# Kernel optimization log

Hardware: AMD Instinct MI355X
Metric: run time of the kernel (lower is better)

Reference implementation:

```python
import jax, jax.numpy as jnp
import numpy as np

B, N, D, H, F = 2, 2048, 1024, 16, 4096
HD = D // H


def setup_inputs() -> dict:
    key = jax.random.key(0)
    ks = jax.random.split(key, 16)
    s = 0.02
    x = jax.random.normal(ks[0], (B, N, D), jnp.float32)
    # tail padding: lengths in [N//2, N]; position >= length is padded
    lengths = jax.random.randint(ks[1], (B,), N // 2, N + 1)
    key_padding_mask = jnp.arange(N)[None, :] >= lengths[:, None]  # [B,N] bool, True = pad
    return {
        "x": x,
        "key_padding_mask": key_padding_mask,
        "ln1_g": jnp.ones((D,), jnp.float32),
        "ln1_b": jnp.zeros((D,), jnp.float32),
        "w_in": jax.random.normal(ks[2], (3 * D, D), jnp.float32) * s,  # packed QKV in_proj
        "b_in": jnp.zeros((3 * D,), jnp.float32),
        "w_out": jax.random.normal(ks[3], (D, D), jnp.float32) * s,
        "b_out": jnp.zeros((D,), jnp.float32),
        "ln2_g": jnp.ones((D,), jnp.float32),
        "ln2_b": jnp.zeros((D,), jnp.float32),
        "w1": jax.random.normal(ks[4], (F, D), jnp.float32) * s,
        "b1": jnp.zeros((F,), jnp.float32),
        "w2": jax.random.normal(ks[5], (D, F), jnp.float32) * s,
        "b2": jnp.zeros((D,), jnp.float32),
    }


def _layernorm(x, g, b):
    # source LayerNorm forces fp32 then casts back
    xf = x.astype(jnp.float32)
    m = xf.mean(-1, keepdims=True)
    v = xf.var(-1, keepdims=True)
    return (((xf - m) * jax.lax.rsqrt(v + 1e-5)) * g + b).astype(x.dtype)


def _quick_gelu(x):
    return x * jax.nn.sigmoid(1.702 * x)


def _block(x, key_padding_mask, ln1_g, ln1_b, w_in, b_in, w_out, b_out,
           ln2_g, ln2_b, w1, b1, w2, b2):
    n = x.shape[1]
    # combined mask: causal OR key-pad, with diagonal unmasked for padded query rows
    causal = jnp.triu(jnp.ones((n, n), bool), 1)                      # [N,N]
    combined = causal[None] | key_padding_mask[:, None, :]            # [B,N,N]
    diag = jnp.eye(n, dtype=bool)
    combined = combined & ~(diag[None] & key_padding_mask[:, :, None])

    # --- attention (pre-norm) ---
    xn = _layernorm(x, ln1_g, ln1_b)
    qkv = xn @ w_in.T + b_in                                          # [B,N,3D]
    q, k, v = jnp.split(qkv, 3, axis=-1)
    def heads(t):
        return t.reshape(x.shape[0], n, H, HD).transpose(0, 2, 1, 3)  # [B,H,N,hd]
    q, k, v = heads(q), heads(k), heads(v)
    scores = jnp.einsum('bhqd,bhkd->bhqk', q, k) / np.sqrt(HD)        # [B,H,N,N]
    scores = jnp.where(combined[:, None], -jnp.inf, scores)
    probs = jax.nn.softmax(scores, axis=-1)                           # [B,H,N,N]
    attn = jnp.einsum('bhqk,bhkd->bqhd', probs, v).reshape(x.shape[0], n, D)
    attn = attn @ w_out.T + b_out
    attn = jnp.where(key_padding_mask[:, :, None], 0.0, attn)         # zero padded queries
    weights = probs.mean(axis=1)                                      # need_weights avg over heads

    x = x + attn
    # --- FFN (pre-norm) ---
    xn = _layernorm(x, ln2_g, ln2_b)
    mlp = _quick_gelu(xn @ w1.T + b1) @ w2.T + b2
    x = x + mlp
    return x, weights


def reference(x, key_padding_mask, ln1_g, ln1_b, w_in, b_in, w_out, b_out,
              ln2_g, ln2_b, w1, b1, w2, b2):
    return _block(x, key_padding_mask, ln1_g, ln1_b, w_in, b_in, w_out, b_out,
                  ln2_g, ln2_b, w1, b1, w2, b2)
```

## Files before the change

### kernel.cpp

```cpp
#include <hip/hip_runtime.h>
#include <hip/hip_bf16.h>
#include <stdint.h>

#define DEVI __device__ __forceinline__

typedef __attribute__((ext_vector_type(8)))  short bf16x8;
typedef __attribute__((ext_vector_type(4)))  short s16x4;
typedef __attribute__((ext_vector_type(4)))  float f32x4;
typedef __attribute__((ext_vector_type(16))) float f32x16;
typedef __attribute__((ext_vector_type(2)))  unsigned int u32x2;
typedef __attribute__((ext_vector_type(4)))  unsigned int u32x4;

#define L2E 1.44269504088896f

DEVI unsigned short f2bf(float f){
  union{float f; unsigned int u;} v; v.f = f;
  unsigned int u = v.u;
  u = u + 0x7FFFu + ((u >> 16) & 1u);
  return (unsigned short)(u >> 16);
}

DEVI unsigned int cvt_pk_bf16(float lo, float hi){
  unsigned int r;
  asm("v_cvt_pk_bf16_f32 %0, %1, %2" : "=v"(r) : "v"(lo), "v"(hi));
  return r;
}

typedef const __attribute__((address_space(1))) unsigned int gq_t;
typedef __attribute__((address_space(3))) unsigned int lq_t;

DEVI void gl_lds16(const unsigned short* g, unsigned short* l){
  __builtin_amdgcn_global_load_lds((gq_t*)(uintptr_t)g, (lq_t*)(uintptr_t)l, 16, 0, 0);
}

__global__ void prep_len(const unsigned char* mask, int* lens){
  __shared__ int nz, cnt0, cnt1;
  int tid = threadIdx.x;
  if(tid == 0){ nz = 0; cnt0 = 0; cnt1 = 0; }
  __syncthreads();
  int loc = 0;
  for(int i = tid; i < 4096; i += 256) loc |= mask[i];
  if(loc) atomicOr(&nz, 1);
  __syncthreads();
  bool isu8 = (nz != 0);
  const int* m32 = (const int*)mask;
  int c0 = 0, c1 = 0;
  for(int i = tid; i < 2048; i += 256){
    int p0 = isu8 ? (int)mask[i]        : m32[i];
    int p1 = isu8 ? (int)mask[2048 + i] : m32[2048 + i];
    c0 += (p0 == 0);
    c1 += (p1 == 0);
  }
  atomicAdd(&cnt0, c0);
  atomicAdd(&cnt1, c1);
  __syncthreads();
  if(tid == 0){ lens[0] = cnt0; lens[1] = cnt1; }
}

__global__ void conv_bf16(const float* s, unsigned short* d, int n4){
  int i = blockIdx.x * 256 + threadIdx.x;
  if(i >= n4) return;
  f32x4 v = *(const f32x4*)(s + (size_t)i*4);
  s16x4 o;
  o[0]=(short)f2bf(v[0]); o[1]=(short)f2bf(v[1]);
  o[2]=(short)f2bf(v[2]); o[3]=(short)f2bf(v[3]);
  *(s16x4*)(d + (size_t)i*4) = o;
}

__global__ __launch_bounds__(256)
void ln_k(const float* x, const float* g, const float* b, unsigned short* y){
  int row = blockIdx.x, tid = threadIdx.x;
  const float* xr = x + (size_t)row*1024;
  f32x4 v = *(const f32x4*)(xr + tid*4);
  float s = v[0]+v[1]+v[2]+v[3];
#pragma unroll
  for(int o=1;o<64;o<<=1) s += __shfl_xor(s, o, 64);
  __shared__ float red[8];
  if((tid & 63) == 0) red[tid>>6] = s;
  __syncthreads();
  float mean = (red[0]+red[1]+red[2]+red[3]) * 0.0009765625f;
  float d0=v[0]-mean, d1=v[1]-mean, d2=v[2]-mean, d3=v[3]-mean;
  float s2 = d0*d0 + d1*d1 + d2*d2 + d3*d3;
#pragma unroll
  for(int o=1;o<64;o<<=1) s2 += __shfl_xor(s2, o, 64);
  if((tid & 63) == 0) red[4 + (tid>>6)] = s2;
  __syncthreads();
  float var = (red[4]+red[5]+red[6]+red[7]) * 0.0009765625f;
  float rstd = rsqrtf(var + 1e-5f);
  f32x4 gg = *(const f32x4*)(g + tid*4);
  f32x4 bb = *(const f32x4*)(b + tid*4);
  s16x4 o;
  o[0] = (short)f2bf(d0*rstd*gg[0] + bb[0]);
  o[1] = (short)f2bf(d1*rstd*gg[1] + bb[1]);
  o[2] = (short)f2bf(d2*rstd*gg[2] + bb[2]);
  o[3] = (short)f2bf(d3*rstd*gg[3] + bb[3]);
  *(s16x4*)(y + (size_t)row*1024 + tid*4) = o;
}

struct GemmP {
  const unsigned short* Wt;
  const unsigned short* Xa;
  int Nmat, K;
  const float* bias;
  const float* resid;
  const int* lens;
  float* outF;
  unsigned short* outB;
};

template<int EPI, int NB, int KB>
__global__ __launch_bounds__(256)
void gemm_k(GemmP p){
  constexpr int NF = NB/32;
  constexpr int CPR = KB/8;
  constexpr int NW = (NB*KB)/2048;
  constexpr int NX = (128*KB)/2048;
  __shared__ unsigned short lw[NB*KB];
  __shared__ unsigned short lx[128*KB];
  int nbn = p.Nmat / NB;
  int id = blockIdx.x;
  int cpx = gridDim.x >> 3;
  id = (id & 7)*cpx + (id >> 3);
  int bm = id / nbn, bn = id % nbn;
  int tid = threadIdx.x, lane = tid & 63, g = lane >> 4, l15 = lane & 15;
  int wave = tid >> 6, wm = wave & 1, wn = wave >> 1;

  const unsigned short* srcW[NW]; const unsigned short* srcX[NX];
  unsigned short* dstW[NW]; unsigned short* dstX[NX];
#pragma unroll
  for(int i=0;i<NW;++i){
    int slot = i*256 + tid, row = slot/CPR, c = slot%CPR, cs = c ^ (row & 7);
    srcW[i] = p.Wt + (size_t)(bn*NB + row)*p.K + cs*8;
    dstW[i] = lw + (i*256 + (tid & 192))*8;
  }
#pragma unroll
  for(int i=0;i<NX;++i){
    int slot = i*256 + tid, row = slot/CPR, c = slot%CPR, cs = c ^ (row & 7);
    srcX[i] = p.Xa + (size_t)(bm*128 + row)*p.K + cs*8;
    dstX[i] = lx + (i*256 + (tid & 192))*8;
  }

  f32x4 acc[NF][4];
#pragma unroll
  for(int a=0;a<NF;++a)
#pragma unroll
    for(int bb=0;bb<4;++bb)
#pragma unroll
      for(int e=0;e<4;++e) acc[a][bb][e] = 0.f;

  int iters = p.K / KB;
  for(int kt=0; kt<iters; ++kt){
#pragma unroll
    for(int i=0;i<NW;++i){
      gl_lds16(srcW[i], dstW[i]);
      srcW[i] += KB;
    }
#pragma unroll
    for(int i=0;i<NX;++i){
      gl_lds16(srcX[i], dstX[i]);
      srcX[i] += KB;
    }
    __syncthreads();
#pragma unroll
    for(int kc=0;kc<KB/32;++kc){
      bf16x8 af[NF], bfr[4];
#pragma unroll
      for(int nf=0;nf<NF;++nf){
        int row = wn*(16*NF) + nf*16 + l15;
        int ch = (kc*4 + g) ^ (row & 7);
        af[nf] = *(const bf16x8*)(lw + row*KB + ch*8);
      }
#pragma unroll
      for(int mf=0;mf<4;++mf){
        int row = wm*64 + mf*16 + l15;
        int ch = (kc*4 + g) ^ (row & 7);
        bfr[mf] = *(const bf16x8*)(lx + row*KB + ch*8);
      }
#pragma unroll
      for(int nf=0;nf<NF;++nf)
#pragma unroll
        for(int mf=0;mf<4;++mf)
          acc[nf][mf] = __builtin_amdgcn_mfma_f32_16x16x32_bf16(af[nf], bfr[mf], acc[nf][mf], 0, 0, 0);
    }
    __syncthreads();
  }

#pragma unroll
  for(int mf=0;mf<4;++mf){
    int m = bm*128 + wm*64 + mf*16 + l15;
#pragma unroll
    for(int nf=0;nf<NF;++nf){
      int n = bn*NB + wn*(16*NF) + nf*16 + g*4;
      f32x4 v = acc[nf][mf];
      f32x4 bz = *(const f32x4*)(p.bias + n);
      v = v + bz;
      if constexpr(EPI == 0){
        float sc = (n < 1024) ? 0.125f*L2E : 1.0f;
        s16x4 o;
#pragma unroll
        for(int e=0;e<4;++e) o[e] = (short)f2bf(v[e]*sc);
        *(s16x4*)(p.outB + (size_t)m*p.Nmat + n) = o;
      } else if constexpr(EPI == 1){
        int b_ = m >> 11, q = m & 2047;
        f32x4 r = *(const f32x4*)(p.resid + (size_t)m*1024 + n);
        if(q >= p.lens[b_]){ v[0]=0.f; v[1]=0.f; v[2]=0.f; v[3]=0.f; }
        v = v + r;
        *(f32x4*)(p.outF + (size_t)m*p.Nmat + n) = v;
      } else if constexpr(EPI == 2){
        s16x4 o;
#pragma unroll
        for(int e=0;e<4;++e){
          float sg = v[e]*__builtin_amdgcn_rcpf(1.f + exp2f(-1.702f*L2E*v[e]));
          o[e] = (short)f2bf(sg);
        }
        *(s16x4*)(p.outB + (size_t)m*p.Nmat + n) = o;
      } else {
        f32x4 r = *(const f32x4*)(p.resid + (size_t)m*p.Nmat + n);
        v = v + r;
        *(f32x4*)(p.outF + (size_t)m*p.Nmat + n) = v;
      }
    }
  }
}

__global__ __launch_bounds__(256)
void repack_vt(const unsigned short* qkv, unsigned short* vt){
  __shared__ unsigned short t[64*80];
  int id = blockIdx.x;
  int bh = id >> 5, nt = id & 31;
  int b = bh >> 4, h = bh & 15;
  int tid = threadIdx.x;
  int r = tid >> 2, c0 = (tid & 3)*16;
  const unsigned short* src = qkv + ((size_t)(b*2048 + nt*64 + r)*3072 + 2048 + h*64 + c0);
  bf16x8 v0 = *(const bf16x8*)(src);
  bf16x8 v1 = *(const bf16x8*)(src + 8);
  *(bf16x8*)(t + r*80 + c0) = v0;
  *(bf16x8*)(t + r*80 + c0 + 8) = v1;
  __syncthreads();
#pragma unroll
  for(int cc=0; cc<2; ++cc){
    int ci = cc*256 + tid;
    int hd = ci >> 3, nc = (ci & 7)*8;
    bf16x8 o;
#pragma unroll
    for(int i=0;i<8;++i) o[i] = (short)t[(nc+i)*80 + hd];
    *(bf16x8*)(vt + ((size_t)(bh*64 + hd)*2048 + nt*64 + nc)) = o;
  }
}

__global__ __launch_bounds__(256)
void attn_flash(const unsigned short* qkv, const unsigned short* vt,
                unsigned short* attnO, float* mrow, float* lrow, const int* lens)
{
  __shared__ unsigned short lk[3][64*64];
  __shared__ unsigned short lv[3][64*64];
  int id = blockIdx.x;
  int jj = id & 255;
  int bh = jj & 31;
  int qt = (id < 256) ? (15 - (jj >> 5)) : (jj >> 5);
  int b = bh >> 4, h = bh & 15;
  int tid = threadIdx.x, lane = tid & 63, wave = tid >> 6;
  int hi = lane >> 5, l31 = lane & 31;
  int q = qt*128 + wave*32 + l31;
  int len_b = lens[b];

  const unsigned short* qptr = qkv + ((size_t)(b*2048 + q)*3072 + h*64);
  bf16x8 qf[4];
#pragma unroll
  for(int ks=0;ks<4;++ks) qf[ks] = *(const bf16x8*)(qptr + ks*16 + hi*8);
  asm volatile("" :: "v"(qf[0]), "v"(qf[1]), "v"(qf[2]), "v"(qf[3]), "s"(len_b));

  const unsigned short* srcK[2]; const unsigned short* srcV[2];
  int dof[2];
#pragma unroll
  for(int i=0;i<2;++i){
    int slot = i*256 + tid, row = slot >> 3, c = slot & 7, cs = c ^ (row & 7);
    srcK[i] = qkv + ((size_t)(b*2048 + row)*3072 + 1024 + h*64) + cs*8;
    srcV[i] = vt + ((size_t)(bh*64 + row)*2048) + cs*8;
    dof[i] = (i*256 + (tid & 192))*8;
  }

  f32x16 oacc[2];
#pragma unroll
  for(int a=0;a<2;++a)
#pragma unroll
    for(int e=0;e<16;++e) oacc[a][e] = 0.f;
  float mcur = -1e30f, lsum = 0.f;
  int ktmax = qt*2 + 1;

#pragma unroll
  for(int i=0;i<2;++i){
    gl_lds16(srcK[i], &lk[0][dof[i]]);
    gl_lds16(srcV[i], &lv[0][dof[i]]);
    srcK[i] += (size_t)64*3072;
    srcV[i] += 64;
  }

  int buf = 0;
  for(int kt=0; kt<=ktmax; ++kt){
    int nb = buf + 1; if(nb == 3) nb = 0;
    if(kt < ktmax){
#pragma unroll
      for(int i=0;i<2;++i){
        gl_lds16(srcK[i], &lk[nb][dof[i]]);
        gl_lds16(srcV[i], &lv[nb][dof[i]]);
        srcK[i] += (size_t)64*3072;
        srcV[i] += 64;
      }
      asm volatile("s_waitcnt vmcnt(4)" ::: "memory");
    } else {
      asm volatile("s_waitcnt vmcnt(0)" ::: "memory");
    }
    asm volatile("s_barrier" ::: "memory");

    f32x16 s2[2];
    __builtin_amdgcn_s_setprio(1);
#pragma unroll
    for(int kb=0;kb<2;++kb){
      f32x16 a;
#pragma unroll
      for(int e=0;e<16;++e) a[e] = 0.f;
      int row = kb*32 + l31;
#pragma unroll
      for(int ks=0;ks<4;++ks){
        int ch = (ks*2 + hi) ^ (row & 7);
        bf16x8 kf = *(const bf16x8*)(&lk[buf][0] + row*64 + ch*8);
        a = __builtin_amdgcn_mfma_f32_32x32x16_bf16(kf, qf[ks], a, 0, 0, 0);
      }
      s2[kb] = a;
    }
    __builtin_amdgcn_s_setprio(0);

    float tmax = -1e30f;
    bool full = (kt*64 + 63 < qt*128 + wave*32) && (kt*64 + 64 <= len_b);
    if(full){
#pragma unroll
      for(int kb=0;kb<2;++kb)
#pragma unroll
        for(int r=0;r<16;++r)
          tmax = fmaxf(tmax, s2[kb][r]);
    } else {
#pragma unroll
      for(int kb=0;kb<2;++kb)
#pragma unroll
        for(int r=0;r<16;++r){
          int key = kt*64 + kb*32 + (r&3) + 8*(r>>2) + 4*hi;
          bool ok = (key == q) || ((key < q) && (key < len_b));
          float tv = ok ? s2[kb][r] : -1e30f;
          s2[kb][r] = tv;
          tmax = fmaxf(tmax, tv);
        }
    }
    tmax = fmaxf(tmax, __shfl_xor(tmax, 32, 64));

    if(!__all(tmax <= mcur + 8.f)){
      float mnew = fmaxf(mcur, tmax);
      float fsc = exp2f(mcur - mnew);
      lsum *= fsc;
#pragma unroll
      for(int a=0;a<2;++a)
#pragma unroll
        for(int e=0;e<16;++e) oacc[a][e] *= fsc;
      mcur = mnew;
    }
    float rsum = 0.f;
#pragma unroll
    for(int kb=0;kb<2;++kb)
#pragma unroll
      for(int r=0;r<16;++r){
        float pv = exp2f(s2[kb][r] - mcur);
        s2[kb][r] = pv;
        rsum += pv;
      }
    rsum += __shfl_xor(rsum, 32, 64);
    lsum += rsum;

    __builtin_amdgcn_s_setprio(1);
#pragma unroll
    for(int ks=0;ks<4;++ks){
      int kb = ks >> 1, r0 = (ks & 1)*8;
      unsigned int a0 = cvt_pk_bf16(s2[kb][r0+0], s2[kb][r0+1]);
      unsigned int a1 = cvt_pk_bf16(s2[kb][r0+2], s2[kb][r0+3]);
      unsigned int a2 = cvt_pk_bf16(s2[kb][r0+4], s2[kb][r0+5]);
      unsigned int a3 = cvt_pk_bf16(s2[kb][r0+6], s2[kb][r0+7]);
      unsigned int b0 = __shfl_xor(a0, 32, 64);
      unsigned int b1 = __shfl_xor(a1, 32, 64);
      unsigned int b2 = __shfl_xor(a2, 32, 64);
      unsigned int b3 = __shfl_xor(a3, 32, 64);
      union { u32x4 u; bf16x8 s8; } pw;
      pw.u[0] = hi ? b2 : a0;
      pw.u[1] = hi ? b3 : a1;
      pw.u[2] = hi ? a2 : b0;
      pw.u[3] = hi ? a3 : b1;
#pragma unroll
      for(int af=0;af<2;++af){
        int vrow = af*32 + l31;
        int ch = (ks*2 + hi) ^ (vrow & 7);
        bf16x8 vf = *(const bf16x8*)(&lv[buf][0] + vrow*64 + ch*8);
        oacc[af] = __builtin_amdgcn_mfma_f32_32x32x16_bf16(vf, pw.s8, oacc[af], 0, 0, 0);
      }
    }
    __builtin_amdgcn_s_setprio(0);
    buf = nb;
  }

  float rl = __builtin_amdgcn_rcpf(lsum);
  if(hi == 0){
    mrow[(size_t)bh*2048 + q] = mcur;
    lrow[(size_t)bh*2048 + q] = lsum;
  }
  unsigned short* obase = attnO + ((size_t)(b*2048 + q)*1024 + h*64);
#pragma unroll
  for(int af=0;af<2;++af)
#pragma unroll
    for(int grp=0; grp<4; ++grp){
      int hd0 = af*32 + grp*8 + hi*4;
      u32x2 st;
      st[0] = cvt_pk_bf16(oacc[af][grp*4+0]*rl, oacc[af][grp*4+1]*rl);
      st[1] = cvt_pk_bf16(oacc[af][grp*4+2]*rl, oacc[af][grp*4+3]*rl);
      *(u32x2*)(obase + hd0) = st;
    }
}

__global__ void prep_c(const float* mrow, const float* lrow, float* cbuf){
  int i = blockIdx.x*256 + threadIdx.x;
  cbuf[i] = exp2f(-mrow[i]) * __builtin_amdgcn_rcpf(lrow[i]);
}

__global__ __launch_bounds__(256)
void attn_weights(const unsigned short* qkv, const float* cbuf,
                  float* wout, const int* lens)
{
  int id = blockIdx.x;
  int kt = id & 15, qt = (id >> 4) & 15, b = id >> 8;
  int tid = threadIdx.x;
  float* wtile = wout + ((size_t)(b*2048 + qt*128))*2048 + kt*128;

  if(kt > qt){
    f32x4 z; z[0]=0.f; z[1]=0.f; z[2]=0.f; z[3]=0.f;
#pragma unroll
    for(int i=0;i<8;++i){
      float* p = wtile + (size_t)(i*16 + (tid>>4))*2048 + (tid&15)*8;
      *(f32x4*)p = z; *(f32x4*)(p+4) = z;
    }
    return;
  }

  __shared__ unsigned short lk[2][128*64];
  __shared__ unsigned short lq[2][128*64];
  int lane = tid & 63, wave = tid >> 6, hi = lane >> 5, l31 = lane & 31;
  int len_b = lens[b];
  int q_abs = qt*128 + wave*32 + l31;

  const float* cb = cbuf + (size_t)(b*16)*2048 + q_abs;
  float ccs[16];
#pragma unroll
  for(int h=0;h<16;++h) ccs[h] = cb[(size_t)h*2048];

  const unsigned short* srcK[4]; const unsigned short* srcQ[4]; int dA[4];
#pragma unroll
  for(int i=0;i<4;++i){
    int d = i*256 + tid, row = d >> 3, c = d & 7, cs = c ^ (row & 7);
    srcK[i] = qkv + ((size_t)(b*2048 + kt*128 + row)*3072 + 1024) + cs*8;
    srcQ[i] = qkv + ((size_t)(b*2048 + qt*128 + row)*3072) + cs*8;
    dA[i] = d*8;
  }

  float wacc[4][16];
#pragma unroll
  for(int ksub=0;ksub<4;++ksub)
#pragma unroll
    for(int r=0;r<16;++r) wacc[ksub][r] = 0.f;

#pragma unroll
  for(int i=0;i<4;++i){
    gl_lds16(srcK[i], &lk[0][dA[i]]);
    gl_lds16(srcQ[i], &lq[0][dA[i]]);
  }
  __syncthreads();

  int buf = 0;
  for(int h=0;h<16;++h){
    if(h < 15){
#pragma unroll
      for(int i=0;i<4;++i){
        gl_lds16(srcK[i] + (h+1)*64, &lk[buf^1][dA[i]]);
        gl_lds16(srcQ[i] + (h+1)*64, &lq[buf^1][dA[i]]);
      }
    }
    bf16x8 qf[4];
#pragma unroll
    for(int ks=0;ks<4;++ks){
      int row = wave*32 + l31;
      int ch = (ks*2 + hi) ^ (row & 7);
      qf[ks] = *(const bf16x8*)(&lq[buf][0] + row*64 + ch*8);
    }
    float cc = ccs[h];
#pragma unroll
    for(int ksub=0;ksub<4;++ksub){
      f32x16 sc;
#pragma unroll
      for(int e=0;e<16;++e) sc[e] = 0.f;
#pragma unroll
      for(int ks=0;ks<4;++ks){
        int row = ksub*32 + l31;
        int ch = (ks*2 + hi) ^ (row & 7);
        bf16x8 kf = *(const bf16x8*)(&lk[buf][0] + row*64 + ch*8);
        sc = __builtin_amdgcn_mfma_f32_32x32x16_bf16(kf, qf[ks], sc, 0, 0, 0);
      }
#pragma unroll
      for(int r=0;r<16;++r)
        wacc[ksub][r] += exp2f(sc[r]) * cc;
    }
    __syncthreads();
    buf ^= 1;
  }

#pragma unroll
  for(int ksub=0;ksub<4;++ksub)
#pragma unroll
    for(int rg=0;rg<4;++rg){
      f32x4 v;
#pragma unroll
      for(int e=0;e<4;++e){
        int key_abs = kt*128 + ksub*32 + rg*8 + hi*4 + e;
        bool ok = (key_abs == q_abs) || ((key_abs < q_abs) && (key_abs < len_b));
        v[e] = ok ? wacc[ksub][rg*4 + e]*0.0625f : 0.f;
      }
      *(f32x4*)(wtile + (size_t)(wave*32 + l31)*2048 + ksub*32 + rg*8 + hi*4) = v;
    }
}

extern "C" void kernel_launch(void* const* d_in, const int* in_sizes, int n_in,
                              void* d_out, int out_size, void* d_ws, size_t ws_size,
                              hipStream_t stream)
{
  const float* x     = (const float*)d_in[0];
  const unsigned char* mask = (const unsigned char*)d_in[1];
  const float* ln1g  = (const float*)d_in[2];
  const float* ln1b  = (const float*)d_in[3];
  const float* w_in  = (const float*)d_in[4];
  const float* b_in  = (const float*)d_in[5];
  const float* w_out = (const float*)d_in[6];
  const float* b_out = (const float*)d_in[7];
  const float* ln2g  = (const float*)d_in[8];
  const float* ln2b  = (const float*)d_in[9];
  const float* w1    = (const float*)d_in[10];
  const float* b1    = (const float*)d_in[11];
  const float* w2    = (const float*)d_in[12];
  const float* b2    = (const float*)d_in[13];
  float* out = (float*)d_out;

  char* ws = (char*)d_ws;
  size_t off = 0;
  auto take = [&](size_t bytes)->char*{
    char* p = ws + off; off += (bytes + 255) & ~(size_t)255; return p;
  };
  int* lens            = (int*)take(256);
  unsigned short* wq   = (unsigned short*)take((size_t)3072*1024*2);
  unsigned short* wo   = (unsigned short*)take((size_t)1024*1024*2);
  unsigned short* w1c  = (unsigned short*)take((size_t)4096*1024*2);
  unsigned short* w2c  = (unsigned short*)take((size_t)1024*4096*2);
  unsigned short* xn   = (unsigned short*)take((size_t)4096*1024*2);
  unsigned short* qkv  = (unsigned short*)take((size_t)4096*3072*2);
  unsigned short* vt   = (unsigned short*)take((size_t)32*64*2048*2);
  float* mrow          = (float*)take((size_t)32*2048*4);
  float* lrow          = (float*)take((size_t)32*2048*4);
  float* cbuf          = (float*)take((size_t)32*2048*4);
  unsigned short* aO   = (unsigned short*)take((size_t)4096*1024*2);
  float* x1            = (float*)take((size_t)4096*1024*4);
  unsigned short* hmid = (unsigned short*)take((size_t)4096*4096*2);

  prep_len<<<1,256,0,stream>>>(mask, lens);
  conv_bf16<<<3072,256,0,stream>>>(w_in, wq, 786432);
  conv_bf16<<<1024,256,0,stream>>>(w_out, wo, 262144);
  conv_bf16<<<4096,256,0,stream>>>(w1, w1c, 1048576);
  conv_bf16<<<4096,256,0,stream>>>(w2, w2c, 1048576);
  ln_k<<<4096,256,0,stream>>>(x, ln1g, ln1b, xn);

  GemmP p1{wq, xn, 3072, 1024, b_in, nullptr, nullptr, nullptr, qkv};
  gemm_k<0,128,64><<<768,256,0,stream>>>(p1);
  repack_vt<<<1024,256,0,stream>>>(qkv, vt);
  attn_flash<<<512,256,0,stream>>>(qkv, vt, aO, mrow, lrow, lens);
  prep_c<<<256,256,0,stream>>>(mrow, lrow, cbuf);
  attn_weights<<<512,256,0,stream>>>(qkv, cbuf, out + 4194304, lens);

  GemmP p2{wo, aO, 1024, 1024, b_out, x, lens, x1, nullptr};
  gemm_k<1,64,128><<<512,256,0,stream>>>(p2);
  ln_k<<<4096,256,0,stream>>>(x1, ln2g, ln2b, xn);
  GemmP p3{w1c, xn, 4096, 1024, b1, nullptr, nullptr, nullptr, hmid};
  gemm_k<2,128,64><<<1024,256,0,stream>>>(p3);
  GemmP p4{w2c, hmid, 1024, 4096, b2, x1, nullptr, out, nullptr};
  gemm_k<3,64,128><<<512,256,0,stream>>>(p4);
}
```

Measured before the change: 323.8 us.

## Software-pipeline attention loop: overlap QK^T of next tile with softmax/PV of previous

Restructures the flash attention inner loop so the QK^T MFMAs for key tile t are issued before the softmax and PV work for tile t-1, letting matrix and vector work interleave within a wave. LDS ring buffers grow from 3 to 4 stages so the V tile of t-1 stays valid while t+1 is being loaded. The row max and row sum reductions are split into four independent accumulators to shorten dependency chains, and the setprio hints are dropped. In exchange, live registers go up (two score tiles held at once) and LDS use rises, which may lower occupancy.

```diff
diff --git a/kernel.cpp b/kernel.cpp
--- a/kernel.cpp
+++ b/kernel.cpp
@@ -248,12 +248,92 @@
   }
 }
 
+#define FINISH(TT) do{ \
+  int tt = (TT); \
+  float m0=-1e30f,m1=-1e30f,m2=-1e30f,m3=-1e30f; \
+  bool full_ = (tt*64 + 63 < qt*128 + wave*32) && (tt*64 + 64 <= len_b); \
+  if(full_){ \
+    _Pragma("unroll") \
+    for(int kb=0;kb<2;++kb){ \
+      _Pragma("unroll") \
+      for(int r=0;r<16;r+=4){ \
+        m0=fmaxf(m0,sP[kb][r+0]); m1=fmaxf(m1,sP[kb][r+1]); \
+        m2=fmaxf(m2,sP[kb][r+2]); m3=fmaxf(m3,sP[kb][r+3]); \
+      } \
+    } \
+  } else { \
+    _Pragma("unroll") \
+    for(int kb=0;kb<2;++kb){ \
+      _Pragma("unroll") \
+      for(int r=0;r<16;++r){ \
+        int key = tt*64 + kb*32 + (r&3) + 8*(r>>2) + 4*hi; \
+        bool ok = (key == q) || ((key < q) && (key < len_b)); \
+        float tv = ok ? sP[kb][r] : -1e30f; \
+        sP[kb][r] = tv; \
+        if((r&3)==0) m0=fmaxf(m0,tv); else if((r&3)==1) m1=fmaxf(m1,tv); \
+        else if((r&3)==2) m2=fmaxf(m2,tv); else m3=fmaxf(m3,tv); \
+      } \
+    } \
+  } \
+  float tmax = fmaxf(fmaxf(m0,m1),fmaxf(m2,m3)); \
+  tmax = fmaxf(tmax, __shfl_xor(tmax, 32, 64)); \
+  if(!__all(tmax <= mcur + 8.f)){ \
+    float mnew = fmaxf(mcur, tmax); \
+    float fsc = exp2f(mcur - mnew); \
+    lsum *= fsc; \
+    _Pragma("unroll") \
+    for(int a=0;a<2;++a){ \
+      _Pragma("unroll") \
+      for(int e=0;e<16;++e) oacc[a][e] *= fsc; \
+    } \
+    mcur = mnew; \
+  } \
+  float r0=0.f,r1=0.f,r2=0.f,r3=0.f; \
+  _Pragma("unroll") \
+  for(int kb=0;kb<2;++kb){ \
+    _Pragma("unroll") \
+    for(int r=0;r<16;++r){ \
+      float pv = exp2f(sP[kb][r] - mcur); \
+      sP[kb][r] = pv; \
+      if((r&3)==0) r0+=pv; else if((r&3)==1) r1+=pv; \
+      else if((r&3)==2) r2+=pv; else r3+=pv; \
+    } \
+  } \
+  float rsum = (r0+r1)+(r2+r3); \
+  rsum += __shfl_xor(rsum, 32, 64); \
+  lsum += rsum; \
+  _Pragma("unroll") \
+  for(int ks=0;ks<4;++ks){ \
+    int kb = ks >> 1, q0_ = (ks & 1)*8; \
+    unsigned int a0 = cvt_pk_bf16(sP[kb][q0_+0], sP[kb][q0_+1]); \
+    unsigned int a1 = cvt_pk_bf16(sP[kb][q0_+2], sP[kb][q0_+3]); \
+    unsigned int a2 = cvt_pk_bf16(sP[kb][q0_+4], sP[kb][q0_+5]); \
+    unsigned int a3 = cvt_pk_bf16(sP[kb][q0_+6], sP[kb][q0_+7]); \
+    unsigned int b0 = __shfl_xor(a0, 32, 64); \
+    unsigned int b1 = __shfl_xor(a1, 32, 64); \
+    unsigned int b2 = __shfl_xor(a2, 32, 64); \
+    unsigned int b3 = __shfl_xor(a3, 32, 64); \
+    union { u32x4 u; bf16x8 s8; } pw; \
+    pw.u[0] = hi ? b2 : a0; \
+    pw.u[1] = hi ? b3 : a1; \
+    pw.u[2] = hi ? a2 : b0; \
+    pw.u[3] = hi ? a3 : b1; \
+    _Pragma("unroll") \
+    for(int af=0;af<2;++af){ \
+      int vrow = af*32 + l31; \
+      int ch = (ks*2 + hi) ^ (vrow & 7); \
+      bf16x8 vf = *(const bf16x8*)(&lv[tt&3][0] + vrow*64 + ch*8); \
+      oacc[af] = __builtin_amdgcn_mfma_f32_32x32x16_bf16(vf, pw.s8, oacc[af], 0, 0, 0); \
+    } \
+  } \
+}while(0)
+
 __global__ __launch_bounds__(256)
 void attn_flash(const unsigned short* qkv, const unsigned short* vt,
                 unsigned short* attnO, float* mrow, float* lrow, const int* lens)
 {
-  __shared__ unsigned short lk[3][64*64];
-  __shared__ unsigned short lv[3][64*64];
+  __shared__ unsigned short lk[4][64*64];
+  __shared__ unsigned short lv[4][64*64];
   int id = blockIdx.x;
   int jj = id & 255;
   int bh = jj & 31;
@@ -296,112 +376,42 @@
     srcV[i] += 64;
   }
 
-  int buf = 0;
-  for(int kt=0; kt<=ktmax; ++kt){
-    int nb = buf + 1; if(nb == 3) nb = 0;
-    if(kt < ktmax){
-#pragma unroll
-      for(int i=0;i<2;++i){
-        gl_lds16(srcK[i], &lk[nb][dof[i]]);
-        gl_lds16(srcV[i], &lv[nb][dof[i]]);
-        srcK[i] += (size_t)64*3072;
-        srcV[i] += 64;
-      }
-      asm volatile("s_waitcnt vmcnt(4)" ::: "memory");
-    } else {
-      asm volatile("s_waitcnt vmcnt(0)" ::: "memory");
-    }
-    asm volatile("s_barrier" ::: "memory");
-
-    f32x16 s2[2];
-    __builtin_amdgcn_s_setprio(1);
-#pragma unroll
-    for(int kb=0;kb<2;++kb){
-      f32x16 a;
-#pragma unroll
-      for(int e=0;e<16;++e) a[e] = 0.f;
-      int row = kb*32 + l31;
-#pragma unroll
-      for(int ks=0;ks<4;++ks){
-        int ch = (ks*2 + hi) ^ (row & 7);
-        bf16x8 kf = *(const bf16x8*)(&lk[buf][0] + row*64 + ch*8);
-        a = __builtin_amdgcn_mfma_f32_32x32x16_bf16(kf, qf[ks], a, 0, 0, 0);
-      }
-      s2[kb] = a;
-    }
-    __builtin_amdgcn_s_setprio(0);
-
-    float tmax = -1e30f;
-    bool full = (kt*64 + 63 < qt*128 + wave*32) && (kt*64 + 64 <= len_b);
-    if(full){
-#pragma unroll
-      for(int kb=0;kb<2;++kb)
-#pragma unroll
-        for(int r=0;r<16;++r)
-          tmax = fmaxf(tmax, s2[kb][r]);
-    } else {
-#pragma unroll
-      for(int kb=0;kb<2;++kb)
-#pragma unroll
-        for(int r=0;r<16;++r){
-          int key = kt*64 + kb*32 + (r&3) + 8*(r>>2) + 4*hi;
-          bool ok = (key == q) || ((key < q) && (key < len_b));
-          float tv = ok ? s2[kb][r] : -1e30f;
-          s2[kb][r] = tv;
-          tmax = fmaxf(tmax, tv);
+  f32x16 sP[2];
+  for(int t=0; t<=ktmax+1; ++t){
+    if(t <= ktmax){
+      if(t < ktmax){
+#pragma unroll
+        for(int i=0;i<2;++i){
+          gl_lds16(srcK[i], &lk[(t+1)&3][dof[i]]);
+          gl_lds16(srcV[i], &lv[(t+1)&3][dof[i]]);
+          srcK[i] += (size_t)64*3072;
+          srcV[i] += 64;
         }
-    }
-    tmax = fmaxf(tmax, __shfl_xor(tmax, 32, 64));
-
-    if(!__all(tmax <= mcur + 8.f)){
-      float mnew = fmaxf(mcur, tmax);
-      float fsc = exp2f(mcur - mnew);
-      lsum *= fsc;
-#pragma unroll
-      for(int a=0;a<2;++a)
-#pragma unroll
-        for(int e=0;e<16;++e) oacc[a][e] *= fsc;
-      mcur = mnew;
-    }
-    float rsum = 0.f;
-#pragma unroll
-    for(int kb=0;kb<2;++kb)
-#pragma unroll
-      for(int r=0;r<16;++r){
-        float pv = exp2f(s2[kb][r] - mcur);
-        s2[kb][r] = pv;
-        rsum += pv;
-      }
-    rsum += __shfl_xor(rsum, 32, 64);
-    lsum += rsum;
-
-    __builtin_amdgcn_s_setprio(1);
-#pragma unroll
-    for(int ks=0;ks<4;++ks){
-      int kb = ks >> 1, r0 = (ks & 1)*8;
-      unsigned int a0 = cvt_pk_bf16(s2[kb][r0+0], s2[kb][r0+1]);
-      unsigned int a1 = cvt_pk_bf16(s2[kb][r0+2], s2[kb][r0+3]);
-      unsigned int a2 = cvt_pk_bf16(s2[kb][r0+4], s2[kb][r0+5]);
-      unsigned int a3 = cvt_pk_bf16(s2[kb][r0+6], s2[kb][r0+7]);
-      unsigned int b0 = __shfl_xor(a0, 32, 64);
-      unsigned int b1 = __shfl_xor(a1, 32, 64);
-      unsigned int b2 = __shfl_xor(a2, 32, 64);
-      unsigned int b3 = __shfl_xor(a3, 32, 64);
-      union { u32x4 u; bf16x8 s8; } pw;
-      pw.u[0] = hi ? b2 : a0;
-      pw.u[1] = hi ? b3 : a1;
-      pw.u[2] = hi ? a2 : b0;
-      pw.u[3] = hi ? a3 : b1;
-#pragma unroll
-      for(int af=0;af<2;++af){
-        int vrow = af*32 + l31;
-        int ch = (ks*2 + hi) ^ (vrow & 7);
-        bf16x8 vf = *(const bf16x8*)(&lv[buf][0] + vrow*64 + ch*8);
-        oacc[af] = __builtin_amdgcn_mfma_f32_32x32x16_bf16(vf, pw.s8, oacc[af], 0, 0, 0);
-      }
-    }
-    __builtin_amdgcn_s_setprio(0);
-    buf = nb;
+        asm volatile("s_waitcnt vmcnt(4)" ::: "memory");
+      } else {
+        asm volatile("s_waitcnt vmcnt(0)" ::: "memory");
+      }
+      asm volatile("s_barrier" ::: "memory");
+    }
+    f32x16 sC[2];
+    if(t <= ktmax){
+#pragma unroll
+      for(int kb=0;kb<2;++kb){
+        f32x16 a;
+#pragma unroll
+        for(int e=0;e<16;++e) a[e] = 0.f;
+        int row = kb*32 + l31;
+#pragma unroll
+        for(int ks=0;ks<4;++ks){
+          int ch = (ks*2 + hi) ^ (row & 7);
+          bf16x8 kf = *(const bf16x8*)(&lk[t&3][0] + row*64 + ch*8);
+          a = __builtin_amdgcn_mfma_f32_32x32x16_bf16(kf, qf[ks], a, 0, 0, 0);
+        }
+        sC[kb] = a;
+      }
+    }
+    if(t > 0) FINISH(t-1);
+    if(t <= ktmax){ sP[0] = sC[0]; sP[1] = sC[1]; }
   }
 
   float rl = __builtin_amdgcn_rcpf(lsum);
```

After: 331.1 us. 2.2% more time.

## Switch attention K/V staging to double buffering and split max/sum reductions

Applied to the files above, without the earlier changes.

The flash-attention kernel's K/V LDS staging goes from a three-slot ring with explicit vmcnt waits and raw barriers to a two-slot ping-pong buffer. It now synchronises with __syncthreads after the initial load and at the end of each iteration. The s_setprio hints and the empty asm register pin on the Q fragments are removed. The row max and row sum are split across four independent accumulators to shorten the dependency chains. This lowers LDS use, but it shortens the prefetch distance and relies on __syncthreads to wait for the async global-to-LDS loads, so less load latency may be hidden.

```diff
diff --git a/kernel.cpp b/kernel.cpp
--- a/kernel.cpp
+++ b/kernel.cpp
@@ -252,8 +252,8 @@
 void attn_flash(const unsigned short* qkv, const unsigned short* vt,
                 unsigned short* attnO, float* mrow, float* lrow, const int* lens)
 {
-  __shared__ unsigned short lk[3][64*64];
-  __shared__ unsigned short lv[3][64*64];
+  __shared__ unsigned short lk[2][64*64];
+  __shared__ unsigned short lv[2][64*64];
   int id = blockIdx.x;
   int jj = id & 255;
   int bh = jj & 31;
@@ -268,7 +268,6 @@
   bf16x8 qf[4];
 #pragma unroll
   for(int ks=0;ks<4;++ks) qf[ks] = *(const bf16x8*)(qptr + ks*16 + hi*8);
-  asm volatile("" :: "v"(qf[0]), "v"(qf[1]), "v"(qf[2]), "v"(qf[3]), "s"(len_b));
 
   const unsigned short* srcK[2]; const unsigned short* srcV[2];
   int dof[2];
@@ -295,26 +294,21 @@
     srcK[i] += (size_t)64*3072;
     srcV[i] += 64;
   }
+  __syncthreads();
 
   int buf = 0;
   for(int kt=0; kt<=ktmax; ++kt){
-    int nb = buf + 1; if(nb == 3) nb = 0;
     if(kt < ktmax){
 #pragma unroll
       for(int i=0;i<2;++i){
-        gl_lds16(srcK[i], &lk[nb][dof[i]]);
-        gl_lds16(srcV[i], &lv[nb][dof[i]]);
+        gl_lds16(srcK[i], &lk[buf^1][dof[i]]);
+        gl_lds16(srcV[i], &lv[buf^1][dof[i]]);
         srcK[i] += (size_t)64*3072;
         srcV[i] += 64;
       }
-      asm volatile("s_waitcnt vmcnt(4)" ::: "memory");
-    } else {
-      asm volatile("s_waitcnt vmcnt(0)" ::: "memory");
-    }
-    asm volatile("s_barrier" ::: "memory");
+    }
 
     f32x16 s2[2];
-    __builtin_amdgcn_s_setprio(1);
 #pragma unroll
     for(int kb=0;kb<2;++kb){
       f32x16 a;
@@ -329,16 +323,17 @@
       }
       s2[kb] = a;
     }
-    __builtin_amdgcn_s_setprio(0);
-
-    float tmax = -1e30f;
+
+    float m0=-1e30f, m1=-1e30f, m2=-1e30f, m3=-1e30f;
     bool full = (kt*64 + 63 < qt*128 + wave*32) && (kt*64 + 64 <= len_b);
     if(full){
 #pragma unroll
       for(int kb=0;kb<2;++kb)
 #pragma unroll
-        for(int r=0;r<16;++r)
-          tmax = fmaxf(tmax, s2[kb][r]);
+        for(int r=0;r<16;r+=4){
+          m0=fmaxf(m0,s2[kb][r+0]); m1=fmaxf(m1,s2[kb][r+1]);
+          m2=fmaxf(m2,s2[kb][r+2]); m3=fmaxf(m3,s2[kb][r+3]);
+        }
     } else {
 #pragma unroll
       for(int kb=0;kb<2;++kb)
@@ -348,9 +343,11 @@
           bool ok = (key == q) || ((key < q) && (key < len_b));
           float tv = ok ? s2[kb][r] : -1e30f;
           s2[kb][r] = tv;
-          tmax = fmaxf(tmax, tv);
+          if((r&3)==0) m0=fmaxf(m0,tv); else if((r&3)==1) m1=fmaxf(m1,tv);
+          else if((r&3)==2) m2=fmaxf(m2,tv); else m3=fmaxf(m3,tv);
         }
     }
+    float tmax = fmaxf(fmaxf(m0,m1), fmaxf(m2,m3));
     tmax = fmaxf(tmax, __shfl_xor(tmax, 32, 64));
 
     if(!__all(tmax <= mcur + 8.f)){
@@ -363,26 +360,27 @@
         for(int e=0;e<16;++e) oacc[a][e] *= fsc;
       mcur = mnew;
     }
-    float rsum = 0.f;
+    float r0=0.f, r1=0.f, r2=0.f, r3=0.f;
 #pragma unroll
     for(int kb=0;kb<2;++kb)
 #pragma unroll
       for(int r=0;r<16;++r){
         float pv = exp2f(s2[kb][r] - mcur);
         s2[kb][r] = pv;
-        rsum += pv;
-      }
+        if((r&3)==0) r0+=pv; else if((r&3)==1) r1+=pv;
+        else if((r&3)==2) r2+=pv; else r3+=pv;
+      }
+    float rsum = (r0+r1)+(r2+r3);
     rsum += __shfl_xor(rsum, 32, 64);
     lsum += rsum;
 
-    __builtin_amdgcn_s_setprio(1);
 #pragma unroll
     for(int ks=0;ks<4;++ks){
-      int kb = ks >> 1, r0 = (ks & 1)*8;
-      unsigned int a0 = cvt_pk_bf16(s2[kb][r0+0], s2[kb][r0+1]);
-      unsigned int a1 = cvt_pk_bf16(s2[kb][r0+2], s2[kb][r0+3]);
-      unsigned int a2 = cvt_pk_bf16(s2[kb][r0+4], s2[kb][r0+5]);
-      unsigned int a3 = cvt_pk_bf16(s2[kb][r0+6], s2[kb][r0+7]);
+      int kb = ks >> 1, r0i = (ks & 1)*8;
+      unsigned int a0 = cvt_pk_bf16(s2[kb][r0i+0], s2[kb][r0i+1]);
+      unsigned int a1 = cvt_pk_bf16(s2[kb][r0i+2], s2[kb][r0i+3]);
+      unsigned int a2 = cvt_pk_bf16(s2[kb][r0i+4], s2[kb][r0i+5]);
+      unsigned int a3 = cvt_pk_bf16(s2[kb][r0i+6], s2[kb][r0i+7]);
       unsigned int b0 = __shfl_xor(a0, 32, 64);
       unsigned int b1 = __shfl_xor(a1, 32, 64);
       unsigned int b2 = __shfl_xor(a2, 32, 64);
@@ -400,8 +398,8 @@
         oacc[af] = __builtin_amdgcn_mfma_f32_32x32x16_bf16(vf, pw.s8, oacc[af], 0, 0, 0);
       }
     }
-    __builtin_amdgcn_s_setprio(0);
-    buf = nb;
+    __syncthreads();
+    buf ^= 1;
   }
 
   float rl = __builtin_amdgcn_rcpf(lsum);
```

After: 320.0 us. Within noise of the previous version (-1.2%).
